# Kernel tuning notes

Measured on AMD Instinct MI355X. Metric: run time of the kernel, lower is better.

Reference implementation:

```python
import jax, jax.numpy as jnp
import numpy as np

P_DROP = 0.6  # F.dropout default training=True in the original forward

def setup_inputs() -> dict:
    key = jax.random.key(0)
    k1, k2, k3, k4 = jax.random.split(key, 4)
    B, T, V, F, K, O = 32, 12, 1000, 64, 3, 64
    x = jax.random.normal(k1, (B, T, V, F), dtype=jnp.float32)
    Att = jax.random.uniform(k2, (V, V), dtype=jnp.float32)
    cheb = jax.random.normal(k3, (K, V, V), dtype=jnp.float32)   # Chebyshev polynomials T_k(L)
    Theta = jax.random.normal(k4, (K, F, O), dtype=jnp.float32)  # per-order feature transforms
    return {"x": x, "Att": Att, "cheb": cheb, "Theta": Theta}

def reference(x, Att, cheb, Theta):
    # x: [B,T,V,F]; Att: [V,V]; cheb: [K,V,V]; Theta: [K,F,O]
    B, T, V, F = x.shape
    K = cheb.shape[0]
    keep = 1.0 - P_DROP
    # Original draws a fresh dropout mask per (time_step, k); replicate with a fixed key.
    mask = jax.random.bernoulli(jax.random.key(42), keep, (T, K, V, V))
    TkA = cheb * Att                                   # [K,V,V] attention-weighted polynomial
    M = jnp.where(mask, TkA[None] / keep, 0.0)         # [T,K,V,V] inverted dropout
    # rhs = T_k_with_at @ graph_signal, batched over (b,t,k)
    rhs = jnp.einsum('tkuv,btvf->btkuf', M, x)         # [B,T,K,V,F]
    # sum_k rhs_k @ Theta_k  -> [B,T,V,O]; matches permute(0,3,1,2) of stacked outputs
    out = jnp.einsum('btkuf,kfo->btuo', rhs, Theta)
    return jax.nn.relu(out)
```

## Files before the change

### kernel.cpp

```cpp
#include <hip/hip_runtime.h>
#include <hip/hip_bf16.h>
#include <stdint.h>


typedef __attribute__((ext_vector_type(8))) short short8;
typedef __attribute__((ext_vector_type(4))) float f32x4;

__device__ __forceinline__ ushort f2bf(float f) {
  __hip_bfloat16 h = __float2bfloat16(f);
  return *reinterpret_cast<ushort*>(&h);
}

__device__ __forceinline__ void threefry2x32(uint32_t c0, uint32_t c1,
                                             uint32_t& o0, uint32_t& o1) {
  const uint32_t ks0 = 0u;
  const uint32_t ks1 = 42u;
  const uint32_t ks2 = ks0 ^ ks1 ^ 0x1BD11BDAu;
  uint32_t x0 = c0 + ks0;
  uint32_t x1 = c1 + ks1;
#define TFR(r) { x0 += x1; x1 = (x1 << (r)) | (x1 >> (32 - (r))); x1 ^= x0; }
  TFR(13) TFR(15) TFR(26) TFR(6)
  x0 += ks1; x1 += ks2 + 1u;
  TFR(17) TFR(29) TFR(16) TFR(24)
  x0 += ks2; x1 += ks0 + 2u;
  TFR(13) TFR(15) TFR(26) TFR(6)
  x0 += ks0; x1 += ks1 + 3u;
  TFR(17) TFR(29) TFR(16) TFR(24)
  x0 += ks1; x1 += ks2 + 4u;
  TFR(13) TFR(15) TFR(26) TFR(6)
  x0 += ks2; x1 += ks0 + 5u;
#undef TFR
  o0 = x0; o1 = x1;
}

__global__ void build_m(const float* __restrict__ Att,
                        const float* __restrict__ cheb,
                        ushort* __restrict__ Mws) {
  const uint32_t idx = blockIdx.x * 256u + threadIdx.x;
  const uint32_t vp = idx & 1023u;
  const uint32_t up = (idx >> 10) & 1023u;
  const uint32_t tk = idx >> 20;
  float val = 0.f;
  if ((vp < 1000u) & (up < 1000u)) {
    const uint32_t flat = (tk * 1000u + up) * 1000u + vp;
    uint32_t o0, o1;
    threefry2x32(0u, flat, o0, o1);
    const uint32_t bits = o0 ^ o1;
    const float u = __uint_as_float((bits >> 9) | 0x3f800000u) - 1.0f;
    if (u < 0.4f) {
      val = cheb[(tk % 3u) * 1000000u + up * 1000u + vp] *
            Att[up * 1000u + vp] * 2.5f;
    }
  }
  Mws[idx] = f2bf(val);
}

__global__ void transpose_x(const float* __restrict__ x,
                            ushort* __restrict__ xt) {
  __shared__ float lt[64][65];
  const int vc = blockIdx.x, t = blockIdx.y, b = blockIdx.z;
  const int tid = threadIdx.x;
  const int v0 = vc * 64;
#pragma unroll
  for (int i = 0; i < 4; ++i) {
    const int c = i * 256 + tid;
    const int vi = c >> 4, f4 = c & 15;
    float4 q = make_float4(0.f, 0.f, 0.f, 0.f);
    if (v0 + vi < 1000)
      q = *(const float4*)(x + ((((size_t)b * 12 + t) * 1000 + v0 + vi) << 6) + f4 * 4);
    lt[f4 * 4 + 0][vi] = q.x;
    lt[f4 * 4 + 1][vi] = q.y;
    lt[f4 * 4 + 2][vi] = q.z;
    lt[f4 * 4 + 3][vi] = q.w;
  }
  __syncthreads();
  const int f = tid >> 2, g = tid & 3;
  alignas(16) ushort tmp[16];
#pragma unroll
  for (int j = 0; j < 16; ++j) tmp[j] = f2bf(lt[f][g * 16 + j]);
  const size_t base = ((size_t)(t * 2048 + b * 64 + f)) << 10;
  *(uint4*)(xt + base + v0 + g * 16)     = *(const uint4*)&tmp[0];
  *(uint4*)(xt + base + v0 + g * 16 + 8) = *(const uint4*)&tmp[8];
}

#define LDT 72

#define MFMA(a, b, c) __builtin_amdgcn_mfma_f32_16x16x32_bf16((a), (b), (c), 0, 0, 0)

#define LOADCH(R0, R1, R2, R3, R4, R5, R6, R7, R8, R9, VC)                    \
  do {                                                                        \
    const size_t co_ = (size_t)(VC) * 64;                                     \
    R0 = *(const uint4*)(Mws + aS0 + co_);                                    \
    R1 = *(const uint4*)(Mws + aS1 + co_);                                    \
    R2 = *(const uint4*)(Mws + aS2 + co_);                                    \
    R3 = *(const uint4*)(Mws + aS3 + co_);                                    \
    R4 = *(const uint4*)(Mws + aS4 + co_);                                    \
    R5 = *(const uint4*)(Mws + aS5 + co_);                                    \
    R6 = *(const uint4*)(xt + bS0 + co_);                                     \
    R7 = *(const uint4*)(xt + bS1 + co_);                                     \
    R8 = *(const uint4*)(xt + bS2 + co_);                                     \
    R9 = *(const uint4*)(xt + bS3 + co_);                                     \
  } while (0)

#define WRITECH(R0, R1, R2, R3, R4, R5, R6, R7, R8, R9)                       \
  do {                                                                        \
    *(uint4*)&smem[(tid) * 8]                = R0;                            \
    *(uint4*)&smem[(256 + tid) * 8]          = R1;                            \
    *(uint4*)&smem[(512 + tid) * 8]          = R2;                            \
    *(uint4*)&smem[(768 + tid) * 8]          = R3;                            \
    *(uint4*)&smem[(1024 + tid) * 8]         = R4;                            \
    *(uint4*)&smem[(1280 + tid) * 8]         = R5;                            \
    *(uint4*)&smem[12288 + (tid) * 8]        = R6;                            \
    *(uint4*)&smem[12288 + (256 + tid) * 8]  = R7;                            \
    *(uint4*)&smem[12288 + (512 + tid) * 8]  = R8;                            \
    *(uint4*)&smem[12288 + (768 + tid) * 8]  = R9;                            \
  } while (0)

#define BURST()                                                               \
  do {                                                                        \
    _Pragma("unroll")                                                         \
    for (int ks = 0; ks < 2; ++ks) {                                          \
      const int cs_ = (((ks * 4 + quad) ^ rsw)) << 3;                         \
      short8 bv[4];                                                           \
      _Pragma("unroll")                                                       \
      for (int ni = 0; ni < 4; ++ni)                                          \
        bv[ni] = *(const short8*)&smem[12288 +                                \
                     (wn * 64 + ni * 16 + l15) * 64 + cs_];                   \
      _Pragma("unroll")                                                       \
      for (int k = 0; k < 3; ++k) {                                           \
        short8 av[2];                                                         \
        _Pragma("unroll")                                                     \
        for (int mi = 0; mi < 2; ++mi)                                        \
          av[mi] = *(const short8*)&smem[k * 4096 +                           \
                       (wu * 32 + mi * 16 + l15) * 64 + cs_];                 \
        _Pragma("unroll")                                                     \
        for (int mi = 0; mi < 2; ++mi)                                        \
          _Pragma("unroll")                                                   \
          for (int ni = 0; ni < 4; ++ni)                                      \
            pacc[k][mi][ni] = MFMA(av[mi], bv[ni], pacc[k][mi][ni]);          \
      }                                                                       \
    }                                                                         \
  } while (0)

__global__ __launch_bounds__(256, 2)
void cheb_main(const ushort* __restrict__ Mws, const ushort* __restrict__ xt,
               const float* __restrict__ Theta, float* __restrict__ out) {
  __shared__ __align__(16) ushort smem[20480];
  const int tid = threadIdx.x;
  const int lane = tid & 63;
  const int w = tid >> 6;
  const int wu = w >> 1, wn = w & 1;
  const int quad = lane >> 4, l15 = lane & 15;
  const int rsw = l15 & 7;

  const int bid = blockIdx.x;
  const int swz = (bid & 7) * 384 + (bid >> 3);
  const int ut = swz & 15;
  const int g = swz >> 4;
  const int nt = g & 15;
  const int t = g >> 4;
  const int u0 = ut * 64, n0 = nt * 128;

  const size_t mbase = (size_t)(t * 3) << 20;
  const size_t xrow0 = (size_t)(t * 2048 + n0);

  const int rA0 = tid >> 3,           cA0 = (tid & 7) ^ (rA0 & 7);
  const int rA1 = (256 + tid) >> 3 & 63, cA1 = (tid & 7) ^ (rA1 & 7);
  const int rA2 = tid >> 3,           cA2 = cA0;
  const int rA3 = rA1,                cA3 = cA1;
  const int rA4 = tid >> 3,           cA4 = cA0;
  const int rA5 = rA1,                cA5 = cA1;
  const size_t aS0 = mbase + ((size_t)(u0 + rA0) << 10) + cA0 * 8;
  const size_t aS1 = mbase + ((size_t)(u0 + rA1) << 10) + cA1 * 8;
  const size_t aS2 = mbase + (1ull << 20) + ((size_t)(u0 + rA2) << 10) + cA2 * 8;
  const size_t aS3 = mbase + (1ull << 20) + ((size_t)(u0 + rA3) << 10) + cA3 * 8;
  const size_t aS4 = mbase + (2ull << 20) + ((size_t)(u0 + rA4) << 10) + cA4 * 8;
  const size_t aS5 = mbase + (2ull << 20) + ((size_t)(u0 + rA5) << 10) + cA5 * 8;
  const int rB0 = tid >> 3,           cB0 = (tid & 7) ^ (rB0 & 7);
  const int rB1 = (256 + tid) >> 3,   cB1 = (tid & 7) ^ (rB1 & 7);
  const int rB2 = (512 + tid) >> 3,   cB2 = (tid & 7) ^ (rB2 & 7);
  const int rB3 = (768 + tid) >> 3,   cB3 = (tid & 7) ^ (rB3 & 7);
  const size_t bS0 = ((xrow0 + rB0) << 10) + cB0 * 8;
  const size_t bS1 = ((xrow0 + rB1) << 10) + cB1 * 8;
  const size_t bS2 = ((xrow0 + rB2) << 10) + cB2 * 8;
  const size_t bS3 = ((xrow0 + rB3) << 10) + cB3 * 8;

  f32x4 pacc[3][2][4];
#pragma unroll
  for (int k = 0; k < 3; ++k)
#pragma unroll
    for (int i = 0; i < 2; ++i)
#pragma unroll
      for (int j = 0; j < 4; ++j) pacc[k][i][j] = f32x4{0.f, 0.f, 0.f, 0.f};

  uint4 p0, p1, p2, p3, p4, p5, p6, p7, p8, p9;

  LOADCH(p0, p1, p2, p3, p4, p5, p6, p7, p8, p9, 0);
  WRITECH(p0, p1, p2, p3, p4, p5, p6, p7, p8, p9);
  __syncthreads();

#pragma unroll 1
  for (int vc = 0; vc < 16; ++vc) {
    if (vc < 15) LOADCH(p0, p1, p2, p3, p4, p5, p6, p7, p8, p9, vc + 1);
    __builtin_amdgcn_s_setprio(1);
    BURST();
    __builtin_amdgcn_s_setprio(0);
    __syncthreads();
    if (vc < 15) {
      WRITECH(p0, p1, p2, p3, p4, p5, p6, p7, p8, p9);
      __syncthreads();
    }
  }

  ushort* sP  = smem + w * 2304;
  ushort* sTh = smem + 9216;
  f32x4 oacc[2][4];
#pragma unroll
  for (int i = 0; i < 2; ++i)
#pragma unroll
    for (int j = 0; j < 4; ++j) oacc[i][j] = f32x4{0.f, 0.f, 0.f, 0.f};

#pragma unroll
  for (int k = 0; k < 3; ++k) {
    __syncthreads();
#pragma unroll
    for (int mi = 0; mi < 2; ++mi)
#pragma unroll
      for (int ni = 0; ni < 4; ++ni)
#pragma unroll
        for (int r = 0; r < 4; ++r)
          sP[(mi * 16 + quad * 4 + r) * LDT + ni * 16 + l15] = f2bf(pacc[k][mi][ni][r]);
    for (int e = tid; e < 4096; e += 256) {
      const int f = e >> 6, o = e & 63;
      sTh[o * LDT + f] = f2bf(Theta[k * 4096 + e]);
    }
    __syncthreads();
#pragma unroll
    for (int ks = 0; ks < 2; ++ks) {
      short8 a2[2], b2[4];
#pragma unroll
      for (int mi = 0; mi < 2; ++mi)
        a2[mi] = *(const short8*)&sP[(mi * 16 + l15) * LDT + ks * 32 + quad * 8];
#pragma unroll
      for (int ni = 0; ni < 4; ++ni)
        b2[ni] = *(const short8*)&sTh[(ni * 16 + l15) * LDT + ks * 32 + quad * 8];
#pragma unroll
      for (int mi = 0; mi < 2; ++mi)
#pragma unroll
        for (int ni = 0; ni < 4; ++ni)
          oacc[mi][ni] = MFMA(a2[mi], b2[ni], oacc[mi][ni]);
    }
  }

#pragma unroll
  for (int mi = 0; mi < 2; ++mi) {
    const int u_base = u0 + wu * 32 + mi * 16 + quad * 4;
#pragma unroll
    for (int ni = 0; ni < 4; ++ni) {
      const int n = n0 + wn * 64 + ni * 16 + l15;
      const int b = n >> 6, oo = n & 63;
      float* op = out + (((size_t)b * 12 + t) * 1000) * 64 + oo;
#pragma unroll
      for (int r = 0; r < 4; ++r) {
        const int u = u_base + r;
        if (u < 1000) op[(size_t)u * 64] = fmaxf(oacc[mi][ni][r], 0.f);
      }
    }
  }
}

extern "C" void kernel_launch(void* const* d_in, const int* in_sizes, int n_in,
                              void* d_out, int out_size, void* d_ws, size_t ws_size,
                              hipStream_t stream) {
  const float* x     = (const float*)d_in[0];
  const float* Att   = (const float*)d_in[1];
  const float* cheb  = (const float*)d_in[2];
  const float* Theta = (const float*)d_in[3];
  float* out = (float*)d_out;

  ushort* Mws = (ushort*)d_ws;
  ushort* xtw = Mws + 37748736ull;

  build_m<<<147456, 256, 0, stream>>>(Att, cheb, Mws);
  transpose_x<<<dim3(16, 12, 32), 256, 0, stream>>>(x, xtw);
  cheb_main<<<3072, 256, 0, stream>>>(Mws, xtw, Theta, out);
}
```

Measured before the change: 283.4 us.

## Double-buffer LDS in main GEMM loop and merge prep kernels into one launch

The main loop now alternates between two LDS buffers, so the prefetched chunk is written into the idle buffer right after compute. This drops one of the two barriers per chunk. The mask-building and x-transpose kernels are merged into a single launch that picks its role from the block index, removing one kernel launch. LDS per block doubles to 80 KB, which may cut occupancy below the two blocks per CU requested by the launch bounds.

```diff
diff --git a/kernel.cpp b/kernel.cpp
--- a/kernel.cpp
+++ b/kernel.cpp
@@ -33,33 +33,38 @@
   o0 = x0; o1 = x1;
 }
 
-__global__ void build_m(const float* __restrict__ Att,
-                        const float* __restrict__ cheb,
-                        ushort* __restrict__ Mws) {
-  const uint32_t idx = blockIdx.x * 256u + threadIdx.x;
-  const uint32_t vp = idx & 1023u;
-  const uint32_t up = (idx >> 10) & 1023u;
-  const uint32_t tk = idx >> 20;
-  float val = 0.f;
-  if ((vp < 1000u) & (up < 1000u)) {
-    const uint32_t flat = (tk * 1000u + up) * 1000u + vp;
-    uint32_t o0, o1;
-    threefry2x32(0u, flat, o0, o1);
-    const uint32_t bits = o0 ^ o1;
-    const float u = __uint_as_float((bits >> 9) | 0x3f800000u) - 1.0f;
-    if (u < 0.4f) {
-      val = cheb[(tk % 3u) * 1000000u + up * 1000u + vp] *
-            Att[up * 1000u + vp] * 2.5f;
-    }
-  }
-  Mws[idx] = f2bf(val);
-}
-
-__global__ void transpose_x(const float* __restrict__ x,
-                            ushort* __restrict__ xt) {
+__global__ void prep(const float* __restrict__ x,
+                     const float* __restrict__ Att,
+                     const float* __restrict__ cheb,
+                     ushort* __restrict__ Mws,
+                     ushort* __restrict__ xtw) {
   __shared__ float lt[64][65];
-  const int vc = blockIdx.x, t = blockIdx.y, b = blockIdx.z;
+  const int bid = blockIdx.x;
   const int tid = threadIdx.x;
+
+  if (bid >= 6144) {
+    const uint32_t idx = (uint32_t)(bid - 6144) * 256u + tid;
+    const uint32_t vp = idx & 1023u;
+    const uint32_t up = (idx >> 10) & 1023u;
+    const uint32_t tk = idx >> 20;
+    float val = 0.f;
+    if ((vp < 1000u) & (up < 1000u)) {
+      const uint32_t flat = (tk * 1000u + up) * 1000u + vp;
+      uint32_t o0, o1;
+      threefry2x32(0u, flat, o0, o1);
+      const uint32_t bits = o0 ^ o1;
+      const float u = __uint_as_float((bits >> 9) | 0x3f800000u) - 1.0f;
+      if (u < 0.4f) {
+        val = cheb[(tk % 3u) * 1000000u + up * 1000u + vp] *
+              Att[up * 1000u + vp] * 2.5f;
+      }
+    }
+    Mws[idx] = f2bf(val);
+    return;
+  }
+
+  const int r = bid;
+  const int vc = r & 15, t = (r >> 4) % 12, b = r / 192;
   const int v0 = vc * 64;
 #pragma unroll
   for (int i = 0; i < 4; ++i) {
@@ -79,44 +84,43 @@
 #pragma unroll
   for (int j = 0; j < 16; ++j) tmp[j] = f2bf(lt[f][g * 16 + j]);
   const size_t base = ((size_t)(t * 2048 + b * 64 + f)) << 10;
-  *(uint4*)(xt + base + v0 + g * 16)     = *(const uint4*)&tmp[0];
-  *(uint4*)(xt + base + v0 + g * 16 + 8) = *(const uint4*)&tmp[8];
+  *(uint4*)(xtw + base + v0 + g * 16)     = *(const uint4*)&tmp[0];
+  *(uint4*)(xtw + base + v0 + g * 16 + 8) = *(const uint4*)&tmp[8];
 }
 
 #define LDT 72
-
 #define MFMA(a, b, c) __builtin_amdgcn_mfma_f32_16x16x32_bf16((a), (b), (c), 0, 0, 0)
 
-#define LOADCH(R0, R1, R2, R3, R4, R5, R6, R7, R8, R9, VC)                    \
+#define LOADCH(VC)                                                            \
   do {                                                                        \
     const size_t co_ = (size_t)(VC) * 64;                                     \
-    R0 = *(const uint4*)(Mws + aS0 + co_);                                    \
-    R1 = *(const uint4*)(Mws + aS1 + co_);                                    \
-    R2 = *(const uint4*)(Mws + aS2 + co_);                                    \
-    R3 = *(const uint4*)(Mws + aS3 + co_);                                    \
-    R4 = *(const uint4*)(Mws + aS4 + co_);                                    \
-    R5 = *(const uint4*)(Mws + aS5 + co_);                                    \
-    R6 = *(const uint4*)(xt + bS0 + co_);                                     \
-    R7 = *(const uint4*)(xt + bS1 + co_);                                     \
-    R8 = *(const uint4*)(xt + bS2 + co_);                                     \
-    R9 = *(const uint4*)(xt + bS3 + co_);                                     \
+    p0 = *(const uint4*)(Mws + aS0 + co_);                                    \
+    p1 = *(const uint4*)(Mws + aS1 + co_);                                    \
+    p2 = *(const uint4*)(Mws + aS2 + co_);                                    \
+    p3 = *(const uint4*)(Mws + aS3 + co_);                                    \
+    p4 = *(const uint4*)(Mws + aS4 + co_);                                    \
+    p5 = *(const uint4*)(Mws + aS5 + co_);                                    \
+    p6 = *(const uint4*)(xt + bS0 + co_);                                     \
+    p7 = *(const uint4*)(xt + bS1 + co_);                                     \
+    p8 = *(const uint4*)(xt + bS2 + co_);                                     \
+    p9 = *(const uint4*)(xt + bS3 + co_);                                     \
   } while (0)
 
-#define WRITECH(R0, R1, R2, R3, R4, R5, R6, R7, R8, R9)                       \
+#define WRITECH(BP)                                                           \
   do {                                                                        \
-    *(uint4*)&smem[(tid) * 8]                = R0;                            \
-    *(uint4*)&smem[(256 + tid) * 8]          = R1;                            \
-    *(uint4*)&smem[(512 + tid) * 8]          = R2;                            \
-    *(uint4*)&smem[(768 + tid) * 8]          = R3;                            \
-    *(uint4*)&smem[(1024 + tid) * 8]         = R4;                            \
-    *(uint4*)&smem[(1280 + tid) * 8]         = R5;                            \
-    *(uint4*)&smem[12288 + (tid) * 8]        = R6;                            \
-    *(uint4*)&smem[12288 + (256 + tid) * 8]  = R7;                            \
-    *(uint4*)&smem[12288 + (512 + tid) * 8]  = R8;                            \
-    *(uint4*)&smem[12288 + (768 + tid) * 8]  = R9;                            \
+    *(uint4*)&(BP)[(tid) * 8]                = p0;                            \
+    *(uint4*)&(BP)[(256 + tid) * 8]          = p1;                            \
+    *(uint4*)&(BP)[(512 + tid) * 8]          = p2;                            \
+    *(uint4*)&(BP)[(768 + tid) * 8]          = p3;                            \
+    *(uint4*)&(BP)[(1024 + tid) * 8]         = p4;                            \
+    *(uint4*)&(BP)[(1280 + tid) * 8]         = p5;                            \
+    *(uint4*)&(BP)[12288 + (tid) * 8]        = p6;                            \
+    *(uint4*)&(BP)[12288 + (256 + tid) * 8]  = p7;                            \
+    *(uint4*)&(BP)[12288 + (512 + tid) * 8]  = p8;                            \
+    *(uint4*)&(BP)[12288 + (768 + tid) * 8]  = p9;                            \
   } while (0)
 
-#define BURST()                                                               \
+#define BURST(BP)                                                             \
   do {                                                                        \
     _Pragma("unroll")                                                         \
     for (int ks = 0; ks < 2; ++ks) {                                          \
@@ -124,14 +128,14 @@
       short8 bv[4];                                                           \
       _Pragma("unroll")                                                       \
       for (int ni = 0; ni < 4; ++ni)                                          \
-        bv[ni] = *(const short8*)&smem[12288 +                                \
+        bv[ni] = *(const short8*)&(BP)[12288 +                                \
                      (wn * 64 + ni * 16 + l15) * 64 + cs_];                   \
       _Pragma("unroll")                                                       \
       for (int k = 0; k < 3; ++k) {                                           \
         short8 av[2];                                                         \
         _Pragma("unroll")                                                     \
         for (int mi = 0; mi < 2; ++mi)                                        \
-          av[mi] = *(const short8*)&smem[k * 4096 +                           \
+          av[mi] = *(const short8*)&(BP)[k * 4096 +                           \
                        (wu * 32 + mi * 16 + l15) * 64 + cs_];                 \
         _Pragma("unroll")                                                     \
         for (int mi = 0; mi < 2; ++mi)                                        \
@@ -145,13 +149,16 @@
 __global__ __launch_bounds__(256, 2)
 void cheb_main(const ushort* __restrict__ Mws, const ushort* __restrict__ xt,
                const float* __restrict__ Theta, float* __restrict__ out) {
-  __shared__ __align__(16) ushort smem[20480];
+  __shared__ __align__(16) ushort smem[40960];
   const int tid = threadIdx.x;
   const int lane = tid & 63;
   const int w = tid >> 6;
   const int wu = w >> 1, wn = w & 1;
   const int quad = lane >> 4, l15 = lane & 15;
   const int rsw = l15 & 7;
+
+  ushort* buf0 = smem;
+  ushort* buf1 = smem + 20480;
 
   const int bid = blockIdx.x;
   const int swz = (bid & 7) * 384 + (bid >> 3);
@@ -164,22 +171,18 @@
   const size_t mbase = (size_t)(t * 3) << 20;
   const size_t xrow0 = (size_t)(t * 2048 + n0);
 
-  const int rA0 = tid >> 3,           cA0 = (tid & 7) ^ (rA0 & 7);
-  const int rA1 = (256 + tid) >> 3 & 63, cA1 = (tid & 7) ^ (rA1 & 7);
-  const int rA2 = tid >> 3,           cA2 = cA0;
-  const int rA3 = rA1,                cA3 = cA1;
-  const int rA4 = tid >> 3,           cA4 = cA0;
-  const int rA5 = rA1,                cA5 = cA1;
+  const int rA0 = tid >> 3,              cA0 = (tid & 7) ^ (rA0 & 7);
+  const int rA1 = ((256 + tid) >> 3) & 63, cA1 = (tid & 7) ^ (rA1 & 7);
   const size_t aS0 = mbase + ((size_t)(u0 + rA0) << 10) + cA0 * 8;
   const size_t aS1 = mbase + ((size_t)(u0 + rA1) << 10) + cA1 * 8;
-  const size_t aS2 = mbase + (1ull << 20) + ((size_t)(u0 + rA2) << 10) + cA2 * 8;
-  const size_t aS3 = mbase + (1ull << 20) + ((size_t)(u0 + rA3) << 10) + cA3 * 8;
-  const size_t aS4 = mbase + (2ull << 20) + ((size_t)(u0 + rA4) << 10) + cA4 * 8;
-  const size_t aS5 = mbase + (2ull << 20) + ((size_t)(u0 + rA5) << 10) + cA5 * 8;
-  const int rB0 = tid >> 3,           cB0 = (tid & 7) ^ (rB0 & 7);
-  const int rB1 = (256 + tid) >> 3,   cB1 = (tid & 7) ^ (rB1 & 7);
-  const int rB2 = (512 + tid) >> 3,   cB2 = (tid & 7) ^ (rB2 & 7);
-  const int rB3 = (768 + tid) >> 3,   cB3 = (tid & 7) ^ (rB3 & 7);
+  const size_t aS2 = mbase + (1ull << 20) + ((size_t)(u0 + rA0) << 10) + cA0 * 8;
+  const size_t aS3 = mbase + (1ull << 20) + ((size_t)(u0 + rA1) << 10) + cA1 * 8;
+  const size_t aS4 = mbase + (2ull << 20) + ((size_t)(u0 + rA0) << 10) + cA0 * 8;
+  const size_t aS5 = mbase + (2ull << 20) + ((size_t)(u0 + rA1) << 10) + cA1 * 8;
+  const int rB0 = tid >> 3,         cB0 = (tid & 7) ^ (rB0 & 7);
+  const int rB1 = (256 + tid) >> 3, cB1 = (tid & 7) ^ (rB1 & 7);
+  const int rB2 = (512 + tid) >> 3, cB2 = (tid & 7) ^ (rB2 & 7);
+  const int rB3 = (768 + tid) >> 3, cB3 = (tid & 7) ^ (rB3 & 7);
   const size_t bS0 = ((xrow0 + rB0) << 10) + cB0 * 8;
   const size_t bS1 = ((xrow0 + rB1) << 10) + cB1 * 8;
   const size_t bS2 = ((xrow0 + rB2) << 10) + cB2 * 8;
@@ -195,21 +198,25 @@
 
   uint4 p0, p1, p2, p3, p4, p5, p6, p7, p8, p9;
 
-  LOADCH(p0, p1, p2, p3, p4, p5, p6, p7, p8, p9, 0);
-  WRITECH(p0, p1, p2, p3, p4, p5, p6, p7, p8, p9);
+  LOADCH(0);
+  WRITECH(buf0);
   __syncthreads();
 
 #pragma unroll 1
-  for (int vc = 0; vc < 16; ++vc) {
-    if (vc < 15) LOADCH(p0, p1, p2, p3, p4, p5, p6, p7, p8, p9, vc + 1);
+  for (int it = 0; it < 8; ++it) {
+    const int vc = it * 2;
+    if (vc < 15) LOADCH(vc + 1);
     __builtin_amdgcn_s_setprio(1);
-    BURST();
+    BURST(buf0);
     __builtin_amdgcn_s_setprio(0);
-    __syncthreads();
-    if (vc < 15) {
-      WRITECH(p0, p1, p2, p3, p4, p5, p6, p7, p8, p9);
-      __syncthreads();
-    }
+    if (vc < 15) WRITECH(buf1);
+    __syncthreads();
+    if (vc + 1 < 15) LOADCH(vc + 2);
+    __builtin_amdgcn_s_setprio(1);
+    BURST(buf1);
+    __builtin_amdgcn_s_setprio(0);
+    if (vc + 1 < 15) WRITECH(buf0);
+    __syncthreads();
   }
 
   ushort* sP  = smem + w * 2304;
@@ -281,7 +288,6 @@
   ushort* Mws = (ushort*)d_ws;
   ushort* xtw = Mws + 37748736ull;
 
-  build_m<<<147456, 256, 0, stream>>>(Att, cheb, Mws);
-  transpose_x<<<dim3(16, 12, 32), 256, 0, stream>>>(x, xtw);
+  prep<<<153600, 256, 0, stream>>>(x, Att, cheb, Mws, xtw);
   cheb_main<<<3072, 256, 0, stream>>>(Mws, xtw, Theta, out);
 }
```

New measurement: 277.3 us. 2.1% less time.
